# Performance work log

Measured on AMD Instinct MI355X. Metric: run time of the kernel, lower is better.

Reference implementation:

```python
import jax, jax.numpy as jnp
import numpy as np
from jax import lax

WINDOW_SIZE = 11
C1 = 0.01 ** 2
C2 = 0.03 ** 2


def make_window(window_size: int) -> jnp.ndarray:
    # scipy.ndimage.gaussian_filter(np.ones(ws), sigma) with mode='reflect'
    # preserves constant inputs exactly, so gauss_1d == ones(ws).
    # outer(ones, ones) / sum -> uniform box window of weight 1/ws^2.
    return jnp.full((window_size, window_size), 1.0 / (window_size * window_size), dtype=jnp.float32)


def setup_inputs() -> dict:
    key = jax.random.key(0)
    k1, k2 = jax.random.split(key)
    B, C, D, H, W = 1, 1, 64, 512, 512
    x = jax.random.uniform(k1, (B, C, D, H, W), dtype=jnp.float32)
    y = jax.random.uniform(k2, (B, C, D, H, W), dtype=jnp.float32)
    window = make_window(WINDOW_SIZE)
    return {"x": x, "y": y, "window": window}


def _windowed_sum(imgs, window):
    # imgs: [N,1,H,W]; window: [ws,ws]. 'same' cross-correlation (window is symmetric).
    ws = window.shape[0]
    pad = ws // 2
    w = window[None, None, :, :]  # [O=1, I=1, ws, ws]
    return lax.conv_general_dilated(
        imgs, w, window_strides=(1, 1), padding=[(pad, pad), (pad, pad)],
        dimension_numbers=("NCHW", "OIHW", "NCHW"))


def reference(x, y, window):
    B, C, D, H, W = x.shape
    # Fold depth into the conv batch dim: every depth slice is an independent 2D SSIM.
    xs = x.transpose(0, 2, 1, 3, 4).reshape(B * D, C, H, W)
    ys = y.transpose(0, 2, 1, 3, 4).reshape(B * D, C, H, W)
    # Single batched conv over [x, y, x^2, y^2, x*y]
    stacked = jnp.concatenate([xs, ys, xs * xs, ys * ys, xs * ys], axis=0)
    conv = _windowed_sum(stacked, window)
    mu_x, mu_y, e_x2, e_y2, e_xy = jnp.split(conv, 5, axis=0)
    mu_x_sq = mu_x * mu_x
    mu_y_sq = mu_y * mu_y
    mu_xy = mu_x * mu_y
    sigma_x_sq = e_x2 - mu_x_sq
    sigma_y_sq = e_y2 - mu_y_sq
    sigma_xy = e_xy - mu_xy
    ssim_map = ((2.0 * mu_xy + C1) * (2.0 * sigma_xy + C2)) / (
        (mu_x_sq + mu_y_sq + C1) * (sigma_x_sq + sigma_y_sq + C2))
    # Per-slice means averaged over slices == global mean (all slices same size).
    return 1.0 - ssim_map.mean()
```

## Files before the change

### kernel.cpp

```cpp
#include <hip/hip_runtime.h>


constexpr int IMG    = 512;
constexpr int OUT_R  = 22;
constexpr int CHUNKS = (IMG + OUT_R - 1) / OUT_R;
constexpr int ITERS  = (OUT_R + 10) / 4;
constexpr int PW     = 524;
constexpr int PLANE  = 4 * PW;
constexpr float WSCALE = 1.0f / 121.0f;
constexpr float C1F = 1e-4f;
constexpr float C2F = 9e-4f;

__device__ __forceinline__ int sidx(int c) {
  return c ^ (((c >> 5) & 3) << 1);
}

template <bool ATOMIC>
__global__ __launch_bounds__(256, 3) void ssim_main(const float* __restrict__ x,
                                                    const float* __restrict__ y,
                                                    float* __restrict__ out_ws) {
  __shared__ float slab[5 * PLANE];
  __shared__ float wsum[4];

  const int tid   = threadIdx.x;
  const int chunk = blockIdx.x;
  const int z     = blockIdx.y;
  const int O0    = chunk * OUT_R;
  const int r0    = O0 - 5;
  const float* xs = x + (size_t)z * IMG * IMG;
  const float* ys = y + (size_t)z * IMG * IMG;

  if (tid < 240) {
    const int q  = tid / 48;
    const int rj = (tid % 48) / 12;
    const int ci = tid % 12;
    const int c  = (ci < 6) ? ci : (518 + ci - 6);
    slab[q * PLANE + rj * PW + sidx(c)] = 0.f;
  }

  const int c0 = 2 * tid;
  float sX0 = 0.f, sX1 = 0.f, sY0 = 0.f, sY1 = 0.f;
  float sXX0 = 0.f, sXX1 = 0.f, sYY0 = 0.f, sYY1 = 0.f, sXY0 = 0.f, sXY1 = 0.f;

  const int wb = sidx(c0 + 6);

  const int g    = tid & 63;
  const int jrow = tid >> 6;
  int ra[10];
#pragma unroll
  for (int m = 0; m < 10; ++m) ra[m] = jrow * PW + sidx(8 * g + 2 * m);

  float acc = 0.f;

  for (int k = 0; k < ITERS; ++k) {
#pragma unroll
    for (int j = 0; j < 4; ++j) {
      const int gr = r0 + 4 * k + j;
      float2 xn = make_float2(0.f, 0.f), yn = make_float2(0.f, 0.f);
      float2 xo = make_float2(0.f, 0.f), yo = make_float2(0.f, 0.f);
      if ((unsigned)gr < (unsigned)IMG) {
        xn = *(const float2*)(xs + (size_t)gr * IMG + c0);
        yn = *(const float2*)(ys + (size_t)gr * IMG + c0);
      }
      const int gro = gr - 11;
      if (gro >= r0 && (unsigned)gro < (unsigned)IMG) {
        xo = *(const float2*)(xs + (size_t)gro * IMG + c0);
        yo = *(const float2*)(ys + (size_t)gro * IMG + c0);
      }
      sX0  += xn.x - xo.x;               sX1  += xn.y - xo.y;
      sY0  += yn.x - yo.x;               sY1  += yn.y - yo.y;
      sXX0 += xn.x * xn.x - xo.x * xo.x; sXX1 += xn.y * xn.y - xo.y * xo.y;
      sYY0 += yn.x * yn.x - yo.x * yo.x; sYY1 += yn.y * yn.y - yo.y * yo.y;
      sXY0 += xn.x * yn.x - xo.x * yo.x; sXY1 += xn.y * yn.y - xo.y * yo.y;

      *(float2*)&slab[0 * PLANE + j * PW + wb] = make_float2(sX0, sX1);
      *(float2*)&slab[1 * PLANE + j * PW + wb] = make_float2(sY0, sY1);
      *(float2*)&slab[2 * PLANE + j * PW + wb] = make_float2(sXX0, sXX1);
      *(float2*)&slab[3 * PLANE + j * PW + wb] = make_float2(sYY0, sYY1);
      *(float2*)&slab[4 * PLANE + j * PW + wb] = make_float2(sXY0, sXY1);
    }
    __syncthreads();

    const int iw   = 4 * k + jrow;
    const int orow = O0 + iw - 10;
    if (iw >= 10 && orow < IMG) {
      float b[5][8];
#pragma unroll
      for (int q = 0; q < 5; ++q) {
        float v[20];
#pragma unroll
        for (int m = 0; m < 10; ++m) {
          const float2 t = *(const float2*)&slab[q * PLANE + ra[m]];
          v[2 * m] = t.x; v[2 * m + 1] = t.y;
        }
        float s = v[1];
#pragma unroll
        for (int k2 = 2; k2 <= 11; ++k2) s += v[k2];
        b[q][0] = s;
#pragma unroll
        for (int j2 = 1; j2 < 8; ++j2) { s += v[j2 + 11] - v[j2]; b[q][j2] = s; }
      }
#pragma unroll
      for (int j2 = 0; j2 < 8; ++j2) {
        const float mu_x = b[0][j2] * WSCALE;
        const float mu_y = b[1][j2] * WSCALE;
        const float ex2  = b[2][j2] * WSCALE;
        const float ey2  = b[3][j2] * WSCALE;
        const float exy  = b[4][j2] * WSCALE;
        const float mxx = mu_x * mu_x;
        const float myy = mu_y * mu_y;
        const float mxy = mu_x * mu_y;
        const float num = fmaf(2.f, mxy, C1F) * fmaf(2.f, exy - mxy, C2F);
        const float den = (mxx + myy + C1F) * ((ex2 - mxx) + (ey2 - myy) + C2F);
        acc += num * __builtin_amdgcn_rcpf(den);
      }
    }
    __syncthreads();
  }

#pragma unroll
  for (int off = 32; off > 0; off >>= 1) acc += __shfl_down(acc, off, 64);
  if ((tid & 63) == 0) wsum[tid >> 6] = acc;
  __syncthreads();
  if (tid == 0) {
    const float t = wsum[0] + wsum[1] + wsum[2] + wsum[3];
    if (ATOMIC) {
      atomicAdd(out_ws, t);
    } else {
      out_ws[blockIdx.y * CHUNKS + blockIdx.x] = t;
    }
  }
}

__global__ void ssim_finalize(const float* __restrict__ partials, int n,
                              float* __restrict__ out) {
  __shared__ float wsum[4];
  float acc = 0.f;
  for (int i = threadIdx.x; i < n; i += 256) acc += partials[i];
#pragma unroll
  for (int off = 32; off > 0; off >>= 1) acc += __shfl_down(acc, off, 64);
  if ((threadIdx.x & 63) == 0) wsum[threadIdx.x >> 6] = acc;
  __syncthreads();
  if (threadIdx.x == 0) {
    const float t = wsum[0] + wsum[1] + wsum[2] + wsum[3];
    out[0] = 1.0f - t * (1.0f / (64.0f * 512.0f * 512.0f));
  }
}

__global__ void ssim_zero(float* p) {
  if (threadIdx.x == 0) p[0] = 0.f;
}

__global__ void ssim_finalize_atomic(const float* __restrict__ accp,
                                     float* __restrict__ out) {
  if (threadIdx.x == 0)
    out[0] = 1.0f - accp[0] * (1.0f / (64.0f * 512.0f * 512.0f));
}

extern "C" void kernel_launch(void* const* d_in, const int* in_sizes, int n_in,
                              void* d_out, int out_size, void* d_ws, size_t ws_size,
                              hipStream_t stream) {
  const float* x = (const float*)d_in[0];
  const float* y = (const float*)d_in[1];
  float* out = (float*)d_out;

  dim3 grid(CHUNKS, 64);
  dim3 block(256);
  const int nblocks = CHUNKS * 64;

  if (ws_size >= (size_t)nblocks * sizeof(float)) {
    float* partials = (float*)d_ws;
    ssim_main<false><<<grid, block, 0, stream>>>(x, y, partials);
    ssim_finalize<<<1, 256, 0, stream>>>(partials, nblocks, out);
  } else {
    float* accp = (float*)d_ws;
    ssim_zero<<<1, 64, 0, stream>>>(accp);
    ssim_main<true><<<grid, block, 0, stream>>>(x, y, accp);
    ssim_finalize_atomic<<<1, 64, 0, stream>>>(accp, out);
  }
}
```

Baseline: 184.4 us.

## Replace LDS slab with per-wave register bands and shuffle-based horizontal box sum

Each wave now owns an 8-row output band across the full 512-column width. Each lane holds 8 columns of running vertical sums in registers, and the horizontal 11-tap box sum uses cross-lane shuffles instead of LDS reads. This removes shared memory, block-level barriers and the LDS slab traffic. In exchange, every band rereads 10 halo rows, so each input row is loaded about 2.25 times from global memory instead of roughly 1.5 times. Occupancy rises through smaller blocks per wave and launch_bounds set to 4.

```diff
diff --git a/kernel.cpp b/kernel.cpp
--- a/kernel.cpp
+++ b/kernel.cpp
@@ -2,132 +2,144 @@
 
 
 constexpr int IMG    = 512;
-constexpr int OUT_R  = 22;
-constexpr int CHUNKS = (IMG + OUT_R - 1) / OUT_R;
-constexpr int ITERS  = (OUT_R + 10) / 4;
-constexpr int PW     = 524;
-constexpr int PLANE  = 4 * PW;
+constexpr int BAND   = 8;
+constexpr int BANDS  = IMG / BAND;
+constexpr int WPB    = 4;
+constexpr int BX     = BANDS / WPB;
 constexpr float WSCALE = 1.0f / 121.0f;
 constexpr float C1F = 1e-4f;
 constexpr float C2F = 9e-4f;
 
-__device__ __forceinline__ int sidx(int c) {
-  return c ^ (((c >> 5) & 3) << 1);
+__device__ __forceinline__ float shl1(float v, int lane) {
+  const float t = __shfl_up(v, 1, 64);
+  return lane == 0 ? 0.f : t;
+}
+__device__ __forceinline__ float shr1(float v, int lane) {
+  const float t = __shfl_down(v, 1, 64);
+  return lane == 63 ? 0.f : t;
+}
+
+__device__ __forceinline__ void hbox11(const float c[8], int lane, float h[8]) {
+  float w[18];
+  w[0] = shl1(c[3], lane);
+  w[1] = shl1(c[4], lane);
+  w[2] = shl1(c[5], lane);
+  w[3] = shl1(c[6], lane);
+  w[4] = shl1(c[7], lane);
+#pragma unroll
+  for (int k = 0; k < 8; ++k) w[5 + k] = c[k];
+  w[13] = shr1(c[0], lane);
+  w[14] = shr1(c[1], lane);
+  w[15] = shr1(c[2], lane);
+  w[16] = shr1(c[3], lane);
+  w[17] = shr1(c[4], lane);
+  float s = w[0];
+#pragma unroll
+  for (int k = 1; k <= 10; ++k) s += w[k];
+  h[0] = s;
+#pragma unroll
+  for (int j = 1; j < 8; ++j) { s += w[j + 10] - w[j - 1]; h[j] = s; }
 }
 
 template <bool ATOMIC>
-__global__ __launch_bounds__(256, 3) void ssim_main(const float* __restrict__ x,
+__global__ __launch_bounds__(256, 4) void ssim_main(const float* __restrict__ x,
                                                     const float* __restrict__ y,
                                                     float* __restrict__ out_ws) {
-  __shared__ float slab[5 * PLANE];
-  __shared__ float wsum[4];
-
-  const int tid   = threadIdx.x;
-  const int chunk = blockIdx.x;
-  const int z     = blockIdx.y;
-  const int O0    = chunk * OUT_R;
-  const int r0    = O0 - 5;
+  const int tid  = threadIdx.x;
+  const int lane = tid & 63;
+  const int wv   = tid >> 6;
+  const int band = blockIdx.x * WPB + wv;
+  const int z    = blockIdx.y;
+  const int O0   = band * BAND;
+  const int r0   = O0 - 5;
   const float* xs = x + (size_t)z * IMG * IMG;
   const float* ys = y + (size_t)z * IMG * IMG;
+  const int c0   = lane * 8;
 
-  if (tid < 240) {
-    const int q  = tid / 48;
-    const int rj = (tid % 48) / 12;
-    const int ci = tid % 12;
-    const int c  = (ci < 6) ? ci : (518 + ci - 6);
-    slab[q * PLANE + rj * PW + sidx(c)] = 0.f;
-  }
-
-  const int c0 = 2 * tid;
-  float sX0 = 0.f, sX1 = 0.f, sY0 = 0.f, sY1 = 0.f;
-  float sXX0 = 0.f, sXX1 = 0.f, sYY0 = 0.f, sYY1 = 0.f, sXY0 = 0.f, sXY1 = 0.f;
-
-  const int wb = sidx(c0 + 6);
-
-  const int g    = tid & 63;
-  const int jrow = tid >> 6;
-  int ra[10];
-#pragma unroll
-  for (int m = 0; m < 10; ++m) ra[m] = jrow * PW + sidx(8 * g + 2 * m);
-
+  float cX[8]  = {0.f,0.f,0.f,0.f,0.f,0.f,0.f,0.f};
+  float cY[8]  = {0.f,0.f,0.f,0.f,0.f,0.f,0.f,0.f};
+  float cXX[8] = {0.f,0.f,0.f,0.f,0.f,0.f,0.f,0.f};
+  float cYY[8] = {0.f,0.f,0.f,0.f,0.f,0.f,0.f,0.f};
+  float cXY[8] = {0.f,0.f,0.f,0.f,0.f,0.f,0.f,0.f};
   float acc = 0.f;
 
-  for (int k = 0; k < ITERS; ++k) {
+  auto add_row = [&](int gr) {
+    if ((unsigned)gr < (unsigned)IMG) {
+      const float4 a0 = *(const float4*)(xs + (size_t)gr * IMG + c0);
+      const float4 a1 = *(const float4*)(xs + (size_t)gr * IMG + c0 + 4);
+      const float4 b0 = *(const float4*)(ys + (size_t)gr * IMG + c0);
+      const float4 b1 = *(const float4*)(ys + (size_t)gr * IMG + c0 + 4);
+      float vx[8] = {a0.x, a0.y, a0.z, a0.w, a1.x, a1.y, a1.z, a1.w};
+      float vy[8] = {b0.x, b0.y, b0.z, b0.w, b1.x, b1.y, b1.z, b1.w};
 #pragma unroll
-    for (int j = 0; j < 4; ++j) {
-      const int gr = r0 + 4 * k + j;
-      float2 xn = make_float2(0.f, 0.f), yn = make_float2(0.f, 0.f);
-      float2 xo = make_float2(0.f, 0.f), yo = make_float2(0.f, 0.f);
-      if ((unsigned)gr < (unsigned)IMG) {
-        xn = *(const float2*)(xs + (size_t)gr * IMG + c0);
-        yn = *(const float2*)(ys + (size_t)gr * IMG + c0);
-      }
-      const int gro = gr - 11;
-      if (gro >= r0 && (unsigned)gro < (unsigned)IMG) {
-        xo = *(const float2*)(xs + (size_t)gro * IMG + c0);
-        yo = *(const float2*)(ys + (size_t)gro * IMG + c0);
-      }
-      sX0  += xn.x - xo.x;               sX1  += xn.y - xo.y;
-      sY0  += yn.x - yo.x;               sY1  += yn.y - yo.y;
-      sXX0 += xn.x * xn.x - xo.x * xo.x; sXX1 += xn.y * xn.y - xo.y * xo.y;
-      sYY0 += yn.x * yn.x - yo.x * yo.x; sYY1 += yn.y * yn.y - yo.y * yo.y;
-      sXY0 += xn.x * yn.x - xo.x * yo.x; sXY1 += xn.y * yn.y - xo.y * yo.y;
-
-      *(float2*)&slab[0 * PLANE + j * PW + wb] = make_float2(sX0, sX1);
-      *(float2*)&slab[1 * PLANE + j * PW + wb] = make_float2(sY0, sY1);
-      *(float2*)&slab[2 * PLANE + j * PW + wb] = make_float2(sXX0, sXX1);
-      *(float2*)&slab[3 * PLANE + j * PW + wb] = make_float2(sYY0, sYY1);
-      *(float2*)&slab[4 * PLANE + j * PW + wb] = make_float2(sXY0, sXY1);
-    }
-    __syncthreads();
-
-    const int iw   = 4 * k + jrow;
-    const int orow = O0 + iw - 10;
-    if (iw >= 10 && orow < IMG) {
-      float b[5][8];
-#pragma unroll
-      for (int q = 0; q < 5; ++q) {
-        float v[20];
-#pragma unroll
-        for (int m = 0; m < 10; ++m) {
-          const float2 t = *(const float2*)&slab[q * PLANE + ra[m]];
-          v[2 * m] = t.x; v[2 * m + 1] = t.y;
-        }
-        float s = v[1];
-#pragma unroll
-        for (int k2 = 2; k2 <= 11; ++k2) s += v[k2];
-        b[q][0] = s;
-#pragma unroll
-        for (int j2 = 1; j2 < 8; ++j2) { s += v[j2 + 11] - v[j2]; b[q][j2] = s; }
-      }
-#pragma unroll
-      for (int j2 = 0; j2 < 8; ++j2) {
-        const float mu_x = b[0][j2] * WSCALE;
-        const float mu_y = b[1][j2] * WSCALE;
-        const float ex2  = b[2][j2] * WSCALE;
-        const float ey2  = b[3][j2] * WSCALE;
-        const float exy  = b[4][j2] * WSCALE;
-        const float mxx = mu_x * mu_x;
-        const float myy = mu_y * mu_y;
-        const float mxy = mu_x * mu_y;
-        const float num = fmaf(2.f, mxy, C1F) * fmaf(2.f, exy - mxy, C2F);
-        const float den = (mxx + myy + C1F) * ((ex2 - mxx) + (ey2 - myy) + C2F);
-        acc += num * __builtin_amdgcn_rcpf(den);
+      for (int k = 0; k < 8; ++k) {
+        cX[k] += vx[k];
+        cY[k] += vy[k];
+        cXX[k] = fmaf(vx[k], vx[k], cXX[k]);
+        cYY[k] = fmaf(vy[k], vy[k], cYY[k]);
+        cXY[k] = fmaf(vx[k], vy[k], cXY[k]);
       }
     }
-    __syncthreads();
+  };
+  auto sub_row = [&](int gr) {
+    if (gr >= r0 && (unsigned)gr < (unsigned)IMG) {
+      const float4 a0 = *(const float4*)(xs + (size_t)gr * IMG + c0);
+      const float4 a1 = *(const float4*)(xs + (size_t)gr * IMG + c0 + 4);
+      const float4 b0 = *(const float4*)(ys + (size_t)gr * IMG + c0);
+      const float4 b1 = *(const float4*)(ys + (size_t)gr * IMG + c0 + 4);
+      float vx[8] = {a0.x, a0.y, a0.z, a0.w, a1.x, a1.y, a1.z, a1.w};
+      float vy[8] = {b0.x, b0.y, b0.z, b0.w, b1.x, b1.y, b1.z, b1.w};
+#pragma unroll
+      for (int k = 0; k < 8; ++k) {
+        cX[k] -= vx[k];
+        cY[k] -= vy[k];
+        cXX[k] = fmaf(-vx[k], vx[k], cXX[k]);
+        cYY[k] = fmaf(-vy[k], vy[k], cYY[k]);
+        cXY[k] = fmaf(-vx[k], vy[k], cXY[k]);
+      }
+    }
+  };
+  auto emit_row = [&]() {
+    float hX[8], hY[8], hXX[8], hYY[8], hXY[8];
+    hbox11(cX,  lane, hX);
+    hbox11(cY,  lane, hY);
+    hbox11(cXX, lane, hXX);
+    hbox11(cYY, lane, hYY);
+    hbox11(cXY, lane, hXY);
+#pragma unroll
+    for (int j = 0; j < 8; ++j) {
+      const float mu_x = hX[j] * WSCALE;
+      const float mu_y = hY[j] * WSCALE;
+      const float ex2  = hXX[j] * WSCALE;
+      const float ey2  = hYY[j] * WSCALE;
+      const float exy  = hXY[j] * WSCALE;
+      const float mxx = mu_x * mu_x;
+      const float myy = mu_y * mu_y;
+      const float mxy = mu_x * mu_y;
+      const float num = fmaf(2.f, mxy, C1F) * fmaf(2.f, exy - mxy, C2F);
+      const float den = (mxx + myy + C1F) * ((ex2 - mxx) + (ey2 - myy) + C2F);
+      acc += num * __builtin_amdgcn_rcpf(den);
+    }
+  };
+
+  for (int i = 0; i < 10; ++i) add_row(r0 + i);
+
+  add_row(r0 + 10);
+  emit_row();
+
+  for (int i = 11; i < 18; ++i) {
+    add_row(r0 + i);
+    sub_row(r0 + i - 11);
+    emit_row();
   }
 
 #pragma unroll
   for (int off = 32; off > 0; off >>= 1) acc += __shfl_down(acc, off, 64);
-  if ((tid & 63) == 0) wsum[tid >> 6] = acc;
-  __syncthreads();
-  if (tid == 0) {
-    const float t = wsum[0] + wsum[1] + wsum[2] + wsum[3];
+  if (lane == 0) {
     if (ATOMIC) {
-      atomicAdd(out_ws, t);
+      atomicAdd(out_ws, acc);
     } else {
-      out_ws[blockIdx.y * CHUNKS + blockIdx.x] = t;
+      out_ws[(size_t)z * BANDS + band] = acc;
     }
   }
 }
@@ -164,14 +176,14 @@
   const float* y = (const float*)d_in[1];
   float* out = (float*)d_out;
 
-  dim3 grid(CHUNKS, 64);
+  dim3 grid(BX, 64);
   dim3 block(256);
-  const int nblocks = CHUNKS * 64;
+  const int npart = BANDS * 64;
 
-  if (ws_size >= (size_t)nblocks * sizeof(float)) {
+  if (ws_size >= (size_t)npart * sizeof(float)) {
     float* partials = (float*)d_ws;
     ssim_main<false><<<grid, block, 0, stream>>>(x, y, partials);
-    ssim_finalize<<<1, 256, 0, stream>>>(partials, nblocks, out);
+    ssim_finalize<<<1, 256, 0, stream>>>(partials, npart, out);
   } else {
     float* accp = (float*)d_ws;
     ssim_zero<<<1, 64, 0, stream>>>(accp);
```

After: 190.6 us. 1.03x slower.
